# Kernel optimization log

Hardware: AMD Instinct MI355X
Metric: run time of the kernel (lower is better)

## Reference

```python
import jax, jax.numpy as jnp
import numpy as np

NUM_EMBEDDINGS = 512
EMBEDDING_DIM = 64


def setup_inputs() -> dict:
    key = jax.random.key(0)
    k1, k2 = jax.random.split(key)
    z_e = jax.random.normal(k1, (32, EMBEDDING_DIM, 64, 64), dtype=jnp.float32)
    lim = 1.0 / NUM_EMBEDDINGS
    codebook = jax.random.uniform(k2, (NUM_EMBEDDINGS, EMBEDDING_DIM),
                                  dtype=jnp.float32, minval=-lim, maxval=lim)
    return {"z_e": z_e, "codebook": codebook}


def reference(z_e, codebook):
    B, C, H, W = z_e.shape
    # [B,C,H,W] -> [N, C] with N = B*H*W (channels-last flatten)
    z_flat = jnp.transpose(z_e, (0, 2, 3, 1)).reshape(-1, C)
    # squared L2 distance via ||a||^2 + ||b||^2 - 2 a.b (same math, no NxKxC tensor)
    d = (jnp.sum(z_flat * z_flat, axis=1, keepdims=True)          # [N,1]
         + jnp.sum(codebook * codebook, axis=1)[None, :]           # [1,K]
         - 2.0 * jnp.einsum('nc,kc->nk', z_flat, codebook))        # [N,K]
    encoding_indices = jnp.argmin(d, axis=1)                       # [N] int
    z_q = codebook[encoding_indices].reshape(B, H, W, C)
    z_q = jnp.transpose(z_q, (0, 3, 1, 2))                         # [B,C,H,W]
    return z_q, encoding_indices
```

## Files before the change

### kernel.cpp

```cpp
#include <hip/hip_runtime.h>
#include <stdint.h>


#pragma clang fp contract(off)

#define KCODES 512
#define CDIM 64
#define HW 4096
#define ZQ_ELEMS 8388608
#define NPB 256

#define LDS_FLOATS 35584
#define LDS_BYTES  (LDS_FLOATS * 4)

static __device__ __forceinline__ float cnorm_row(const float* __restrict__ row) {
    float r[8];
    #pragma unroll
    for (int j = 0; j < 8; ++j) r[j] = row[j] * row[j];
    #pragma unroll
    for (int i = 8; i < 64; i += 8) {
        #pragma unroll
        for (int j = 0; j < 8; ++j) r[j] = r[j] + row[i + j] * row[i + j];
    }
    return ((r[0] + r[1]) + (r[2] + r[3])) + ((r[4] + r[5]) + (r[6] + r[7]));
}

__global__ void cnorm_kernel(const float* __restrict__ cb,
                             float* __restrict__ cnorm_out) {
    int k = (int)blockIdx.x * 256 + (int)threadIdx.x;
    if (k < KCODES) cnorm_out[k] = cnorm_row(cb + (size_t)k * CDIM);
}

#define QC(Q0,Q1,Q2,Q3,l) \
    ((l) < 4 ? ((l)==0?Q0.x:(l)==1?Q0.y:(l)==2?Q0.z:Q0.w) : \
     (l) < 8 ? ((l)==4?Q1.x:(l)==5?Q1.y:(l)==6?Q1.z:Q1.w) : \
     (l) <12 ? ((l)==8?Q2.x:(l)==9?Q2.y:(l)==10?Q2.z:Q2.w) : \
               ((l)==12?Q3.x:(l)==13?Q3.y:(l)==14?Q3.z:Q3.w))

__global__ __launch_bounds__(1024)
void vq_lds(const float* __restrict__ z_e,
            const float* __restrict__ cb,
            const float* __restrict__ cnorm_g,
            float* __restrict__ out)
{
    extern __shared__ float smem[];
    float* cbs   = smem;
    float* cnorm = smem + 32768;
    float* dcand = smem + 33280;
    int*   kcand = (int*)(smem + 34304);
    int*   kbest = (int*)(smem + 35328);

    const int tid = (int)threadIdx.x;

    {
        const float4* src = (const float4*)cb;
        float4* dst = (float4*)cbs;
        #pragma unroll
        for (int j = 0; j < 8; ++j)
            dst[tid + 1024 * j] = src[tid + 1024 * j];
    }
    if (tid < KCODES)
        cnorm[tid] = cnorm_g ? cnorm_g[tid] : cnorm_row(cb + (size_t)tid * CDIM);

    const int lane = tid & 63;
    const int wid  = __builtin_amdgcn_readfirstlane(tid >> 6);
    const int g    = wid & 3;
    const int pgrp = wid >> 2;

    const int n0 = (int)blockIdx.x * NPB;
    const int b = n0 / HW;
    const int hw0 = n0 % HW;
    const float* zp = z_e + (size_t)b * CDIM * HW + hw0 + pgrp * 64 + lane;

    float zz[CDIM];
    #pragma unroll
    for (int m = 0; m < CDIM; ++m)
        zz[m] = zp[(size_t)m * HW];

    float sz;
    {
        float r[8];
        #pragma unroll
        for (int j = 0; j < 8; ++j) r[j] = zz[j] * zz[j];
        #pragma unroll
        for (int i = 8; i < 64; i += 8) {
            #pragma unroll
            for (int j = 0; j < 8; ++j) r[j] = r[j] + zz[i + j] * zz[i + j];
        }
        sz = ((r[0] + r[1]) + (r[2] + r[3])) + ((r[4] + r[5]) + (r[6] + r[7]));
    }

    __syncthreads();

    float best = 3.4e38f;
    int bk = 0;
    const int k0 = g * 128;

    #pragma unroll 2
    for (int i = 0; i < 128; ++i) {
        const int k = k0 + i;
        const float4* ck4 = (const float4*)(cbs + (size_t)k * CDIM);
        const float An = sz + cnorm[k];

        float4 a0 = ck4[12], a1 = ck4[13], a2 = ck4[14], a3 = ck4[15];
        float4 b0 = ck4[8],  b1 = ck4[9],  b2 = ck4[10], b3 = ck4[11];

        float v[16];
        #pragma unroll
        for (int l = 0; l < 16; ++l)
            v[l] = fmaf(zz[48 + l], QC(a0,a1,a2,a3,l), 0.f);

        a0 = ck4[4]; a1 = ck4[5]; a2 = ck4[6]; a3 = ck4[7];

        #pragma unroll
        for (int l = 0; l < 16; ++l)
            v[l] = fmaf(zz[32 + l], QC(b0,b1,b2,b3,l), v[l]);

        b0 = ck4[0]; b1 = ck4[1]; b2 = ck4[2]; b3 = ck4[3];

        #pragma unroll
        for (int l = 0; l < 16; ++l)
            v[l] = fmaf(zz[16 + l], QC(a0,a1,a2,a3,l), v[l]);

        #pragma unroll
        for (int l = 0; l < 16; ++l)
            v[l] = fmaf(zz[l], QC(b0,b1,b2,b3,l), v[l]);

        float e[8];
        #pragma unroll
        for (int l = 0; l < 8; ++l) e[l] = v[l] + v[8 + l];
        float f[4];
        #pragma unroll
        for (int l = 0; l < 4; ++l) f[l] = e[l] + e[4 + l];
        float g0 = f[0] + f[2];
        float g1 = f[1] + f[3];
        float dot = g0 + g1;

        float d = fmaf(dot, -2.f, An);

        if (d < best) { best = d; bk = k; }
    }

    dcand[g * NPB + pgrp * 64 + lane] = best;
    kcand[g * NPB + pgrp * 64 + lane] = bk;
    __syncthreads();

    if (tid < NPB) {
        float bd = dcand[tid];
        int bi = kcand[tid];
        #pragma unroll
        for (int gg = 1; gg < 4; ++gg) {
            float d2 = dcand[gg * NPB + tid];
            int   k2 = kcand[gg * NPB + tid];
            if (d2 < bd) { bd = d2; bi = k2; }
        }
        out[ZQ_ELEMS + n0 + tid] = (float)bi;
        kbest[tid] = bi;
    }
    __syncthreads();

    const int bi = kbest[pgrp * 64 + lane];
    const float* row = cb + (size_t)bi * CDIM;
    float* op = out + (size_t)b * CDIM * HW + hw0 + pgrp * 64 + lane;
    #pragma unroll
    for (int c = 0; c < 16; ++c) {
        const int ch = g * 16 + c;
        op[(size_t)ch * HW] = row[ch];
    }
}

__global__ __launch_bounds__(256)
void vq_sload(const float* __restrict__ z_e,
              const float* __restrict__ cb,
              const float* __restrict__ cnorm_g,
              float* __restrict__ out)
{
    __shared__ float cnorm[KCODES];
    __shared__ float dcand[4 * 64];
    __shared__ int   kcand[4 * 64];

    if (cnorm_g) {
        #pragma unroll
        for (int k = (int)threadIdx.x; k < KCODES; k += 256)
            cnorm[k] = cnorm_g[k];
    } else {
        for (int k = (int)threadIdx.x; k < KCODES; k += 256)
            cnorm[k] = cnorm_row(cb + (size_t)k * CDIM);
    }

    const int lane = (int)threadIdx.x & 63;
    const int g = __builtin_amdgcn_readfirstlane((int)threadIdx.x >> 6);
    const int n0 = (int)blockIdx.x * 64;
    const int b = n0 / HW;
    const int hw0 = n0 % HW;
    const float* zp = z_e + (size_t)b * CDIM * HW + hw0 + lane;

    float zz[CDIM];
    #pragma unroll
    for (int m = 0; m < CDIM; ++m)
        zz[m] = zp[(size_t)m * HW];

    float sz;
    {
        float r[8];
        #pragma unroll
        for (int j = 0; j < 8; ++j) r[j] = zz[j] * zz[j];
        #pragma unroll
        for (int i = 8; i < 64; i += 8) {
            #pragma unroll
            for (int j = 0; j < 8; ++j) r[j] = r[j] + zz[i + j] * zz[i + j];
        }
        sz = ((r[0] + r[1]) + (r[2] + r[3])) + ((r[4] + r[5]) + (r[6] + r[7]));
    }

    __syncthreads();

    float best = 3.4e38f;
    int bk = 0;
    const int k0 = g * 128;

    for (int i = 0; i < 128; ++i) {
        const int k = k0 + i;
        const float* ck = cb + (size_t)k * CDIM;

        float v[16];
        #pragma unroll
        for (int l = 0; l < 16; ++l)
            v[l] = fmaf(zz[l], ck[l],
                     fmaf(zz[16 + l], ck[16 + l],
                       fmaf(zz[32 + l], ck[32 + l],
                         fmaf(zz[48 + l], ck[48 + l], 0.f))));

        float e[8];
        #pragma unroll
        for (int l = 0; l < 8; ++l) e[l] = v[l] + v[8 + l];
        float f[4];
        #pragma unroll
        for (int l = 0; l < 4; ++l) f[l] = e[l] + e[4 + l];
        float g0 = f[0] + f[2];
        float g1 = f[1] + f[3];
        float dot = g0 + g1;

        float A = sz + cnorm[k];
        float d = fmaf(dot, -2.f, A);

        if (d < best) { best = d; bk = k; }
    }

    dcand[g * 64 + lane] = best;
    kcand[g * 64 + lane] = bk;
    __syncthreads();

    float bd = dcand[lane];
    int bi = kcand[lane];
    #pragma unroll
    for (int gg = 1; gg < 4; ++gg) {
        float d2 = dcand[gg * 64 + lane];
        int   k2 = kcand[gg * 64 + lane];
        if (d2 < bd) { bd = d2; bi = k2; }
    }

    if (g == 0) out[ZQ_ELEMS + n0 + lane] = (float)bi;

    const float* row = cb + (size_t)bi * CDIM;
    float* op = out + (size_t)b * CDIM * HW + hw0 + lane;
    #pragma unroll
    for (int c = 0; c < 16; ++c) {
        const int ch = g * 16 + c;
        op[(size_t)ch * HW] = row[ch];
    }
}

extern "C" void kernel_launch(void* const* d_in, const int* in_sizes, int n_in,
                              void* d_out, int out_size, void* d_ws, size_t ws_size,
                              hipStream_t stream) {
    const float* z_e = (const float*)d_in[0];
    const float* cb  = (const float*)d_in[1];
    float* out = (float*)d_out;

    float* cnorm_ws = nullptr;
    if (ws_size >= KCODES * sizeof(float)) {
        cnorm_ws = (float*)d_ws;
        cnorm_kernel<<<dim3(2), dim3(256), 0, stream>>>(cb, cnorm_ws);
    }

    static int lds_ok = -1;
    if (lds_ok < 0) {
        lds_ok = (hipFuncSetAttribute((const void*)vq_lds,
                                      hipFuncAttributeMaxDynamicSharedMemorySize,
                                      LDS_BYTES) == hipSuccess) ? 1 : 0;
    }

    if (lds_ok == 1) {
        vq_lds<<<dim3(131072 / NPB), dim3(1024), LDS_BYTES, stream>>>(
            z_e, cb, cnorm_ws, out);
    } else {
        vq_sload<<<dim3(2048), dim3(256), 0, stream>>>(z_e, cb, cnorm_ws, out);
    }
}
```

Before: 226.0 us.

## Process two pixels per thread to reuse codebook LDS reads

The LDS-codebook kernel now runs with 512 threads per block instead of 1024, and each thread computes distances for two pixels, 64 apart, against the same codebook rows. Each float4 codebook value read from shared memory feeds two FMA chains, halving LDS traffic per distance computed. In exchange, each thread holds twice as many z values and accumulators, which raises register use and may lower occupancy or cause spills. The z-norm computation is also moved into a helper function.

Result: faster. 212.7 us (-5.9%).

```diff
diff --git a/kernel.cpp b/kernel.cpp
--- a/kernel.cpp
+++ b/kernel.cpp
@@ -31,13 +31,25 @@
     if (k < KCODES) cnorm_out[k] = cnorm_row(cb + (size_t)k * CDIM);
 }
 
+static __device__ __forceinline__ float znorm_pairwise(const float* zz) {
+    float r[8];
+    #pragma unroll
+    for (int j = 0; j < 8; ++j) r[j] = zz[j] * zz[j];
+    #pragma unroll
+    for (int i = 8; i < 64; i += 8) {
+        #pragma unroll
+        for (int j = 0; j < 8; ++j) r[j] = r[j] + zz[i + j] * zz[i + j];
+    }
+    return ((r[0] + r[1]) + (r[2] + r[3])) + ((r[4] + r[5]) + (r[6] + r[7]));
+}
+
 #define QC(Q0,Q1,Q2,Q3,l) \
     ((l) < 4 ? ((l)==0?Q0.x:(l)==1?Q0.y:(l)==2?Q0.z:Q0.w) : \
      (l) < 8 ? ((l)==4?Q1.x:(l)==5?Q1.y:(l)==6?Q1.z:Q1.w) : \
      (l) <12 ? ((l)==8?Q2.x:(l)==9?Q2.y:(l)==10?Q2.z:Q2.w) : \
                ((l)==12?Q3.x:(l)==13?Q3.y:(l)==14?Q3.z:Q3.w))
 
-__global__ __launch_bounds__(1024)
+__global__ __launch_bounds__(512)
 void vq_lds(const float* __restrict__ z_e,
             const float* __restrict__ cb,
             const float* __restrict__ cnorm_g,
@@ -56,8 +68,8 @@
         const float4* src = (const float4*)cb;
         float4* dst = (float4*)cbs;
         #pragma unroll
-        for (int j = 0; j < 8; ++j)
-            dst[tid + 1024 * j] = src[tid + 1024 * j];
+        for (int j = 0; j < 16; ++j)
+            dst[tid + 512 * j] = src[tid + 512 * j];
     }
     if (tid < KCODES)
         cnorm[tid] = cnorm_g ? cnorm_g[tid] : cnorm_row(cb + (size_t)tid * CDIM);
@@ -70,79 +82,99 @@
     const int n0 = (int)blockIdx.x * NPB;
     const int b = n0 / HW;
     const int hw0 = n0 % HW;
-    const float* zp = z_e + (size_t)b * CDIM * HW + hw0 + pgrp * 64 + lane;
-
-    float zz[CDIM];
-    #pragma unroll
-    for (int m = 0; m < CDIM; ++m)
-        zz[m] = zp[(size_t)m * HW];
-
-    float sz;
-    {
-        float r[8];
-        #pragma unroll
-        for (int j = 0; j < 8; ++j) r[j] = zz[j] * zz[j];
-        #pragma unroll
-        for (int i = 8; i < 64; i += 8) {
-            #pragma unroll
-            for (int j = 0; j < 8; ++j) r[j] = r[j] + zz[i + j] * zz[i + j];
-        }
-        sz = ((r[0] + r[1]) + (r[2] + r[3])) + ((r[4] + r[5]) + (r[6] + r[7]));
-    }
-
-    __syncthreads();
-
-    float best = 3.4e38f;
-    int bk = 0;
+    const float* zpa = z_e + (size_t)b * CDIM * HW + hw0 + pgrp * 128 + lane;
+    const float* zpb = zpa + 64;
+
+    float zza[CDIM], zzb[CDIM];
+    #pragma unroll
+    for (int m = 0; m < CDIM; ++m) zza[m] = zpa[(size_t)m * HW];
+    #pragma unroll
+    for (int m = 0; m < CDIM; ++m) zzb[m] = zpb[(size_t)m * HW];
+
+    const float sza = znorm_pairwise(zza);
+    const float szb = znorm_pairwise(zzb);
+
+    __syncthreads();
+
+    float best_a = 3.4e38f, best_b = 3.4e38f;
+    int bk_a = 0, bk_b = 0;
     const int k0 = g * 128;
 
-    #pragma unroll 2
     for (int i = 0; i < 128; ++i) {
         const int k = k0 + i;
         const float4* ck4 = (const float4*)(cbs + (size_t)k * CDIM);
-        const float An = sz + cnorm[k];
-
-        float4 a0 = ck4[12], a1 = ck4[13], a2 = ck4[14], a3 = ck4[15];
-        float4 b0 = ck4[8],  b1 = ck4[9],  b2 = ck4[10], b3 = ck4[11];
-
-        float v[16];
-        #pragma unroll
-        for (int l = 0; l < 16; ++l)
-            v[l] = fmaf(zz[48 + l], QC(a0,a1,a2,a3,l), 0.f);
-
-        a0 = ck4[4]; a1 = ck4[5]; a2 = ck4[6]; a3 = ck4[7];
-
-        #pragma unroll
-        for (int l = 0; l < 16; ++l)
-            v[l] = fmaf(zz[32 + l], QC(b0,b1,b2,b3,l), v[l]);
-
-        b0 = ck4[0]; b1 = ck4[1]; b2 = ck4[2]; b3 = ck4[3];
-
-        #pragma unroll
-        for (int l = 0; l < 16; ++l)
-            v[l] = fmaf(zz[16 + l], QC(a0,a1,a2,a3,l), v[l]);
-
-        #pragma unroll
-        for (int l = 0; l < 16; ++l)
-            v[l] = fmaf(zz[l], QC(b0,b1,b2,b3,l), v[l]);
-
-        float e[8];
-        #pragma unroll
-        for (int l = 0; l < 8; ++l) e[l] = v[l] + v[8 + l];
-        float f[4];
-        #pragma unroll
-        for (int l = 0; l < 4; ++l) f[l] = e[l] + e[4 + l];
-        float g0 = f[0] + f[2];
-        float g1 = f[1] + f[3];
-        float dot = g0 + g1;
-
-        float d = fmaf(dot, -2.f, An);
-
-        if (d < best) { best = d; bk = k; }
-    }
-
-    dcand[g * NPB + pgrp * 64 + lane] = best;
-    kcand[g * NPB + pgrp * 64 + lane] = bk;
+        const float cnk = cnorm[k];
+        const float Ana = sza + cnk;
+        const float Anb = szb + cnk;
+
+        float4 q0 = ck4[12], q1 = ck4[13], q2 = ck4[14], q3 = ck4[15];
+        float4 r0 = ck4[8],  r1 = ck4[9],  r2 = ck4[10], r3 = ck4[11];
+
+        float va[16], vb[16];
+        #pragma unroll
+        for (int l = 0; l < 16; ++l) {
+            const float c = QC(q0,q1,q2,q3,l);
+            va[l] = fmaf(zza[48 + l], c, 0.f);
+            vb[l] = fmaf(zzb[48 + l], c, 0.f);
+        }
+
+        q0 = ck4[4]; q1 = ck4[5]; q2 = ck4[6]; q3 = ck4[7];
+
+        #pragma unroll
+        for (int l = 0; l < 16; ++l) {
+            const float c = QC(r0,r1,r2,r3,l);
+            va[l] = fmaf(zza[32 + l], c, va[l]);
+            vb[l] = fmaf(zzb[32 + l], c, vb[l]);
+        }
+
+        r0 = ck4[0]; r1 = ck4[1]; r2 = ck4[2]; r3 = ck4[3];
+
+        #pragma unroll
+        for (int l = 0; l < 16; ++l) {
+            const float c = QC(q0,q1,q2,q3,l);
+            va[l] = fmaf(zza[16 + l], c, va[l]);
+            vb[l] = fmaf(zzb[16 + l], c, vb[l]);
+        }
+
+        #pragma unroll
+        for (int l = 0; l < 16; ++l) {
+            const float c = QC(r0,r1,r2,r3,l);
+            va[l] = fmaf(zza[l], c, va[l]);
+            vb[l] = fmaf(zzb[l], c, vb[l]);
+        }
+
+        {
+            float e[8];
+            #pragma unroll
+            for (int l = 0; l < 8; ++l) e[l] = va[l] + va[8 + l];
+            float f[4];
+            #pragma unroll
+            for (int l = 0; l < 4; ++l) f[l] = e[l] + e[4 + l];
+            float g0 = f[0] + f[2];
+            float g1 = f[1] + f[3];
+            float dot = g0 + g1;
+            float d = fmaf(dot, -2.f, Ana);
+            if (d < best_a) { best_a = d; bk_a = k; }
+        }
+        {
+            float e[8];
+            #pragma unroll
+            for (int l = 0; l < 8; ++l) e[l] = vb[l] + vb[8 + l];
+            float f[4];
+            #pragma unroll
+            for (int l = 0; l < 4; ++l) f[l] = e[l] + e[4 + l];
+            float g0 = f[0] + f[2];
+            float g1 = f[1] + f[3];
+            float dot = g0 + g1;
+            float d = fmaf(dot, -2.f, Anb);
+            if (d < best_b) { best_b = d; bk_b = k; }
+        }
+    }
+
+    dcand[g * NPB + pgrp * 128 + lane]      = best_a;
+    kcand[g * NPB + pgrp * 128 + lane]      = bk_a;
+    dcand[g * NPB + pgrp * 128 + 64 + lane] = best_b;
+    kcand[g * NPB + pgrp * 128 + 64 + lane] = bk_b;
     __syncthreads();
 
     if (tid < NPB) {
@@ -159,13 +191,17 @@
     }
     __syncthreads();
 
-    const int bi = kbest[pgrp * 64 + lane];
-    const float* row = cb + (size_t)bi * CDIM;
-    float* op = out + (size_t)b * CDIM * HW + hw0 + pgrp * 64 + lane;
+    const int bia = kbest[pgrp * 128 + lane];
+    const int bib = kbest[pgrp * 128 + 64 + lane];
+    const float* rowa = cb + (size_t)bia * CDIM;
+    const float* rowb = cb + (size_t)bib * CDIM;
+    float* opa = out + (size_t)b * CDIM * HW + hw0 + pgrp * 128 + lane;
+    float* opb = opa + 64;
     #pragma unroll
     for (int c = 0; c < 16; ++c) {
         const int ch = g * 16 + c;
-        op[(size_t)ch * HW] = row[ch];
+        opa[(size_t)ch * HW] = rowa[ch];
+        opb[(size_t)ch * HW] = rowb[ch];
     }
 }
 
@@ -200,18 +236,7 @@
     for (int m = 0; m < CDIM; ++m)
         zz[m] = zp[(size_t)m * HW];
 
-    float sz;
-    {
-        float r[8];
-        #pragma unroll
-        for (int j = 0; j < 8; ++j) r[j] = zz[j] * zz[j];
-        #pragma unroll
-        for (int i = 8; i < 64; i += 8) {
-            #pragma unroll
-            for (int j = 0; j < 8; ++j) r[j] = r[j] + zz[i + j] * zz[i + j];
-        }
-        sz = ((r[0] + r[1]) + (r[2] + r[3])) + ((r[4] + r[5]) + (r[6] + r[7]));
-    }
+    float sz = znorm_pairwise(zz);
 
     __syncthreads();
 
@@ -292,7 +317,7 @@
     }
 
     if (lds_ok == 1) {
-        vq_lds<<<dim3(131072 / NPB), dim3(1024), LDS_BYTES, stream>>>(
+        vq_lds<<<dim3(131072 / NPB), dim3(512), LDS_BYTES, stream>>>(
             z_e, cb, cnorm_ws, out);
     } else {
         vq_sload<<<dim3(2048), dim3(256), 0, stream>>>(z_e, cb, cnorm_ws, out);
```
